# Performance work log

Hardware: AMD Instinct MI355X
Metric: run time of the kernel (lower is better)

The kernel has to match this reference:

```python
import jax, jax.numpy as jnp
import numpy as np

N = 65536   # total nodes
E = 1048576 # total edges (avg degree 16)
B = 512     # graphs in batch
H = 4       # gat1 heads
C = 64      # per-head channels / GNN_HIDDEN


def segment_softmax(logits, seg, num_segments):
    # numerically stable softmax over segments (PyG softmax semantics, eps=1e-16)
    m = jax.ops.segment_max(logits, seg, num_segments=num_segments)
    m = jnp.where(jnp.isfinite(m), m, 0.0)
    e = jnp.exp(logits - m[seg])
    s = jax.ops.segment_sum(e, seg, num_segments=num_segments)
    return e / (s[seg] + 1e-16)


def gat_conv(x, edge_index, edge_attr, W, att_src, att_dst, We, att_edge, bias, heads, out_ch, concat):
    # PyG GATConv with edge_dim, add_self_loops=False
    n = x.shape[0]
    h = (x @ W).reshape(n, heads, out_ch)                 # (N,H,C)
    src, dst = edge_index[0], edge_index[1]
    a_s = jnp.sum(h * att_src, axis=-1)                   # (N,H)
    a_d = jnp.sum(h * att_dst, axis=-1)                   # (N,H)
    he = (edge_attr @ We).reshape(-1, heads, out_ch)      # (E,H,C)
    a_e = jnp.sum(he * att_edge, axis=-1)                 # (E,H)
    alpha = jax.nn.leaky_relu(a_s[src] + a_d[dst] + a_e, negative_slope=0.2)
    alpha = segment_softmax(alpha, dst, n)                # softmax over incoming edges per dst
    out = jax.ops.segment_sum(h[src] * alpha[..., None], dst, num_segments=n)  # (N,H,C)
    out = out.reshape(n, heads * out_ch) if concat else out.mean(axis=1)
    return out + bias


def setup_inputs() -> dict:
    key = jax.random.key(0)
    ks = jax.random.split(key, 24)
    s = 0.05
    d = {}
    d["global_feat"] = jax.random.normal(ks[0], (B, 512), jnp.float32)
    d["x"] = jax.random.normal(ks[1], (N, 13), jnp.float32)
    d["roi_feats"] = jax.random.normal(ks[2], (N, 256), jnp.float32)
    d["edge_index"] = jax.random.randint(ks[3], (2, E), 0, N)
    d["edge_attr"] = jax.random.normal(ks[4], (E, 5), jnp.float32)
    d["batch_vec"] = jnp.sort(jax.random.randint(ks[5], (N,), 0, B))
    # roi_proj / scene_proj
    d["roi_W"] = jax.random.normal(ks[6], (256, 64), jnp.float32) * s
    d["roi_b"] = jnp.zeros((64,), jnp.float32)
    d["scene_W"] = jax.random.normal(ks[7], (512, 128), jnp.float32) * s
    d["scene_b"] = jnp.zeros((128,), jnp.float32)
    d["g1_W"] = jax.random.normal(ks[8], (77, H * C), jnp.float32) * s
    d["g1_att_src"] = jax.random.normal(ks[9], (H, C), jnp.float32) * s
    d["g1_att_dst"] = jax.random.normal(ks[10], (H, C), jnp.float32) * s
    d["g1_We"] = jax.random.normal(ks[11], (5, H * C), jnp.float32) * s
    d["g1_att_edge"] = jax.random.normal(ks[12], (H, C), jnp.float32) * s
    d["g1_bias"] = jnp.zeros((H * C,), jnp.float32)
    # gat2: 256 -> 64, 1 head
    d["g2_W"] = jax.random.normal(ks[13], (H * C, C), jnp.float32) * s
    d["g2_att_src"] = jax.random.normal(ks[14], (1, C), jnp.float32) * s
    d["g2_att_dst"] = jax.random.normal(ks[15], (1, C), jnp.float32) * s
    d["g2_We"] = jax.random.normal(ks[16], (5, C), jnp.float32) * s
    d["g2_att_edge"] = jax.random.normal(ks[17], (1, C), jnp.float32) * s
    d["g2_bias"] = jnp.zeros((C,), jnp.float32)
    # attention pooling gate + classifier
    d["gate_W"] = jax.random.normal(ks[18], (C, 1), jnp.float32) * s
    d["gate_b"] = jnp.zeros((1,), jnp.float32)
    d["cls1_W"] = jax.random.normal(ks[19], (128 + C, 64), jnp.float32) * s
    d["cls1_b"] = jnp.zeros((64,), jnp.float32)
    d["cls2_W"] = jax.random.normal(ks[20], (64, 3), jnp.float32) * s
    d["cls2_b"] = jnp.zeros((3,), jnp.float32)
    return d


def reference(global_feat, x, roi_feats, edge_index, edge_attr, batch_vec,
              roi_W, roi_b, scene_W, scene_b,
              g1_W, g1_att_src, g1_att_dst, g1_We, g1_att_edge, g1_bias,
              g2_W, g2_att_src, g2_att_dst, g2_We, g2_att_edge, g2_bias,
              gate_W, gate_b, cls1_W, cls1_b, cls2_W, cls2_b):
    scene = global_feat @ scene_W + scene_b                       # (B,128)
    vis = jax.nn.relu(roi_feats @ roi_W + roi_b)                  # (N,64)
    h = jnp.concatenate([x, vis], axis=-1)                        # (N,77)
    h = jax.nn.relu(gat_conv(h, edge_index, edge_attr, g1_W, g1_att_src, g1_att_dst, g1_We, g1_att_edge, g1_bias, H, C, True))
    h = gat_conv(h, edge_index, edge_attr, g2_W, g2_att_src, g2_att_dst, g2_We, g2_att_edge, g2_bias, 1, C, False)  # (N,64)
    # GlobalAttention pooling
    gate = segment_softmax((h @ gate_W + gate_b)[:, 0], batch_vec, B)
    rel = jax.ops.segment_sum(gate[:, None] * h, batch_vec, num_segments=B)  # (B,64)
    comb = jnp.concatenate([scene, rel], axis=-1)                 # (B,192)
    hid = jax.nn.relu(comb @ cls1_W + cls1_b)                     # dropout off (eval)
    return hid @ cls2_W + cls2_b                                  # (B,3)
```

## Files before the change

kernel.cpp:

```cpp
#include <hip/hip_runtime.h>

#define N_NODES 65536
#define N_EDGES 1048576
#define NB      512

typedef unsigned short u16;
typedef unsigned int   u32;
typedef unsigned long long u64;

__device__ __forceinline__ float bf2f(u16 u) { return __uint_as_float(((u32)u) << 16); }
__device__ __forceinline__ float lo16(u32 u) { return __uint_as_float(u << 16); }
__device__ __forceinline__ float hi16(u32 u) { return __uint_as_float(u & 0xffff0000u); }
__device__ __forceinline__ u16 f2bf(float f) {
    u32 u = __float_as_uint(f);
    u32 r = (u + 0x7fffu + ((u >> 16) & 1u)) >> 16;
    return (u16)r;
}
__device__ __forceinline__ float wsum(float v) {
    for (int o = 32; o; o >>= 1) v += __shfl_xor(v, o, 64);
    return v;
}
__device__ __forceinline__ float wmax(float v) {
    for (int o = 32; o; o >>= 1) v = fmaxf(v, __shfl_xor(v, o, 64));
    return v;
}

__global__ void k_prep(const float* g1We, const float* g1ae, const float* g2We, const float* g2ae,
                       float* M1, float* M2) {
    int t = threadIdx.x;
    if (t < 20) {
        int j = t >> 2, h = t & 3;
        float s = 0.f;
        for (int c = 0; c < 64; c++) s += g1We[j * 256 + h * 64 + c] * g1ae[h * 64 + c];
        M1[t] = s;
    } else if (t < 25) {
        int j = t - 20;
        float s = 0.f;
        for (int c = 0; c < 64; c++) s += g2We[j * 64 + c] * g2ae[c];
        M2[j] = s;
    }
}

__global__ __launch_bounds__(256) void k_scene(const float* __restrict__ gf, const float* __restrict__ W,
                                               const float* __restrict__ bias, float* __restrict__ scene) {
    int idx = blockIdx.x * 256 + threadIdx.x;
    int b = idx >> 7, j = idx & 127;
    float acc = 0.f;
    for (int k = 0; k < 512; k++) acc += gf[b * 512 + k] * W[k * 128 + j];
    scene[idx] = acc + bias[j];
}

__global__ __launch_bounds__(256) void k_hist(const int* ei, int* cnt) {
    int e = blockIdx.x * 256 + threadIdx.x;
    atomicAdd(&cnt[ei[N_EDGES + e]], 1);
}

__global__ __launch_bounds__(256) void k_scan_blk(const int* __restrict__ cnt, int* __restrict__ pre,
                                                  int* __restrict__ bsum) {
    __shared__ int sd[256];
    int t = threadIdx.x, b = blockIdx.x;
    int base = b * 1024 + t * 4;
    int4 c = *(const int4*)(cnt + base);
    int s = c.x + c.y + c.z + c.w;
    sd[t] = s;
    __syncthreads();
    for (int off = 1; off < 256; off <<= 1) {
        int v = (t >= off) ? sd[t - off] : 0;
        __syncthreads();
        sd[t] += v;
        __syncthreads();
    }
    int excl = sd[t] - s;
    int4 p;
    p.x = excl;
    p.y = excl + c.x;
    p.z = excl + c.x + c.y;
    p.w = excl + c.x + c.y + c.z;
    *(int4*)(pre + base) = p;
    if (t == 255) bsum[b] = sd[255];
}

__global__ __launch_bounds__(64) void k_scan_top(int* bsum) {
    int t = threadIdx.x;
    int v = bsum[t];
    int inc = v;
    for (int off = 1; off < 64; off <<= 1) {
        int u = __shfl_up(inc, off, 64);
        if (t >= off) inc += u;
    }
    bsum[t] = inc - v;
}

__global__ __launch_bounds__(256) void k_scan_fix(const int* __restrict__ pre, const int* __restrict__ bsum,
                                                  int* __restrict__ row_ptr, int* __restrict__ coarse_cur) {
    int i = blockIdx.x * 256 + threadIdx.x;
    int v = pre[i] + bsum[i >> 10];
    row_ptr[i] = v;
    if ((i & 255) == 0) coarse_cur[i >> 8] = v;
    if (i == 0) row_ptr[N_NODES] = N_EDGES;
}

__global__ __launch_bounds__(256) void k_bucket(const int* __restrict__ ei, int* coarse_cur,
                                                u32* __restrict__ bpack, int* __restrict__ bsrc) {
    __shared__ u32 stageP[4096];
    __shared__ int stageS[4096];
    __shared__ int bcnt[256], bscan[256], boff[256], gbase[256];
    int t = threadIdx.x;
    int e0 = blockIdx.x * 4096;
    bcnt[t] = 0;
    __syncthreads();
    int dreg[16], sreg[16];
    for (int it = 0; it < 16; it++) {
        int e = e0 + it * 256 + t;
        int dd = ei[N_EDGES + e];
        dreg[it] = dd;
        sreg[it] = ei[e];
        atomicAdd(&bcnt[dd >> 8], 1);
    }
    __syncthreads();
    int v = bcnt[t];
    bscan[t] = v;
    __syncthreads();
    for (int off = 1; off < 256; off <<= 1) {
        int u = (t >= off) ? bscan[t - off] : 0;
        __syncthreads();
        bscan[t] += u;
        __syncthreads();
    }
    boff[t] = bscan[t] - v;
    gbase[t] = v ? atomicAdd(&coarse_cur[t], v) : 0;
    __syncthreads();
    for (int it = 0; it < 16; it++) {
        int e = e0 + it * 256 + t;
        int b = dreg[it] >> 8;
        int pos = atomicAdd(&boff[b], 1);
        stageP[pos] = ((u32)e << 12) | (u32)(dreg[it] & 255);
        stageS[pos] = sreg[it];
    }
    __syncthreads();
    for (int idx = t; idx < 4096; idx += 256) {
        int lo = 0, hi = 255;
        while (lo < hi) { int mid = (lo + hi) >> 1; if (bscan[mid] > idx) hi = mid; else lo = mid + 1; }
        int b = lo;
        int g = gbase[b] + (idx - (bscan[b] - bcnt[b]));
        bpack[g] = stageP[idx];
        bsrc[g] = stageS[idx];
    }
}

__global__ __launch_bounds__(256) void k_sortb(const u32* __restrict__ bpack, const int* __restrict__ bsrc,
                                               const int* __restrict__ row_ptr,
                                               int* __restrict__ eord, int* __restrict__ ssrc) {
    __shared__ int cur[256];
    int t = threadIdx.x, b = blockIdx.x;
    int nbase = b * 256;
    cur[t] = row_ptr[nbase + t];
    __syncthreads();
    int beg = row_ptr[nbase];
    int end = row_ptr[nbase + 256];
    for (int i = beg + t; i < end; i += 256) {
        u32 wd = bpack[i];
        int src = bsrc[i];
        int d8 = wd & 255;
        int pos = atomicAdd(&cur[d8], 1);
        eord[pos] = (int)(wd >> 12);
        ssrc[pos] = src;
    }
}

__global__ __launch_bounds__(256) void k_payload(const int* __restrict__ eord, const float* __restrict__ ea,
                                                 const float* __restrict__ M1, const float* __restrict__ M2,
                                                 float* __restrict__ a1es, float* __restrict__ a2es) {
    int pos = blockIdx.x * 256 + threadIdx.x;
    int e = eord[pos];
    float v[5];
    for (int j = 0; j < 5; j++) v[j] = ea[(size_t)e * 5 + j];
    float4 o;
    o.x = v[0]*M1[0]  + v[1]*M1[4]  + v[2]*M1[8]  + v[3]*M1[12] + v[4]*M1[16];
    o.y = v[0]*M1[1]  + v[1]*M1[5]  + v[2]*M1[9]  + v[3]*M1[13] + v[4]*M1[17];
    o.z = v[0]*M1[2]  + v[1]*M1[6]  + v[2]*M1[10] + v[3]*M1[14] + v[4]*M1[18];
    o.w = v[0]*M1[3]  + v[1]*M1[7]  + v[2]*M1[11] + v[3]*M1[15] + v[4]*M1[19];
    *(float4*)(a1es + (size_t)pos * 4) = o;
    a2es[pos] = v[0]*M2[0] + v[1]*M2[1] + v[2]*M2[2] + v[3]*M2[3] + v[4]*M2[4];
}

__global__ __launch_bounds__(256) void k_vis(const float* __restrict__ A, const float* __restrict__ W,
                                             const float* __restrict__ bias, float* __restrict__ out) {
    __shared__ float At[64][68];
    __shared__ float Wl[64][68];
    int t = threadIdx.x;
    int n0 = blockIdx.x * 64;
    int cg = t & 15, rg = t >> 4;
    int sr = t >> 2, scs = (t & 3) * 16;
    float acc[4][4];
    for (int i = 0; i < 4; i++) for (int j = 0; j < 4; j++) acc[i][j] = 0.f;
    for (int kc = 0; kc < 4; kc++) {
        __syncthreads();
        const float* ap = A + (size_t)(n0 + sr) * 256 + kc * 64 + scs;
        float4 q0 = *(const float4*)ap, q1 = *(const float4*)(ap + 4);
        float4 q2 = *(const float4*)(ap + 8), q3 = *(const float4*)(ap + 12);
        At[scs + 0][sr] = q0.x;  At[scs + 1][sr] = q0.y;  At[scs + 2][sr] = q0.z;  At[scs + 3][sr] = q0.w;
        At[scs + 4][sr] = q1.x;  At[scs + 5][sr] = q1.y;  At[scs + 6][sr] = q1.z;  At[scs + 7][sr] = q1.w;
        At[scs + 8][sr] = q2.x;  At[scs + 9][sr] = q2.y;  At[scs + 10][sr] = q2.z; At[scs + 11][sr] = q2.w;
        At[scs + 12][sr] = q3.x; At[scs + 13][sr] = q3.y; At[scs + 14][sr] = q3.z; At[scs + 15][sr] = q3.w;
        const float* wp = W + (size_t)(kc * 64 + sr) * 64 + scs;
        *(float4*)&Wl[sr][scs + 0]  = *(const float4*)wp;
        *(float4*)&Wl[sr][scs + 4]  = *(const float4*)(wp + 4);
        *(float4*)&Wl[sr][scs + 8]  = *(const float4*)(wp + 8);
        *(float4*)&Wl[sr][scs + 12] = *(const float4*)(wp + 12);
        __syncthreads();
        for (int k = 0; k < 64; k++) {
            float4 a4 = *(const float4*)&At[k][rg * 4];
            float4 w4 = *(const float4*)&Wl[k][cg * 4];
            acc[0][0] += a4.x * w4.x; acc[0][1] += a4.x * w4.y; acc[0][2] += a4.x * w4.z; acc[0][3] += a4.x * w4.w;
            acc[1][0] += a4.y * w4.x; acc[1][1] += a4.y * w4.y; acc[1][2] += a4.y * w4.z; acc[1][3] += a4.y * w4.w;
            acc[2][0] += a4.z * w4.x; acc[2][1] += a4.z * w4.y; acc[2][2] += a4.z * w4.z; acc[2][3] += a4.z * w4.w;
            acc[3][0] += a4.w * w4.x; acc[3][1] += a4.w * w4.y; acc[3][2] += a4.w * w4.z; acc[3][3] += a4.w * w4.w;
        }
    }
    float4 bb = *(const float4*)(bias + cg * 4);
    for (int i = 0; i < 4; i++) {
        float4 o;
        o.x = fmaxf(acc[i][0] + bb.x, 0.f);
        o.y = fmaxf(acc[i][1] + bb.y, 0.f);
        o.z = fmaxf(acc[i][2] + bb.z, 0.f);
        o.w = fmaxf(acc[i][3] + bb.w, 0.f);
        *(float4*)(out + (size_t)(n0 + rg * 4 + i) * 64 + cg * 4) = o;
    }
}

__global__ __launch_bounds__(256) void k_h2(const u16* __restrict__ A, const float* __restrict__ W,
                                            const float* __restrict__ as_, const float* __restrict__ ad_,
                                            u16* __restrict__ out, float* __restrict__ a2s,
                                            float* __restrict__ a2d) {
    __shared__ float At[64][68];
    __shared__ float Wl[64][68];
    int t = threadIdx.x;
    int n0 = blockIdx.x * 64;
    int cg = t & 15, rg = t >> 4;
    int sr = t >> 2, scs = (t & 3) * 16;
    float acc[4][4];
    for (int i = 0; i < 4; i++) for (int j = 0; j < 4; j++) acc[i][j] = 0.f;
    for (int kc = 0; kc < 4; kc++) {
        __syncthreads();
        const u16* ap = A + (size_t)(n0 + sr) * 256 + kc * 64 + scs;
        uint4 u0 = *(const uint4*)ap;
        uint4 u1 = *(const uint4*)(ap + 8);
        At[scs + 0][sr] = lo16(u0.x);  At[scs + 1][sr] = hi16(u0.x);
        At[scs + 2][sr] = lo16(u0.y);  At[scs + 3][sr] = hi16(u0.y);
        At[scs + 4][sr] = lo16(u0.z);  At[scs + 5][sr] = hi16(u0.z);
        At[scs + 6][sr] = lo16(u0.w);  At[scs + 7][sr] = hi16(u0.w);
        At[scs + 8][sr] = lo16(u1.x);  At[scs + 9][sr] = hi16(u1.x);
        At[scs + 10][sr] = lo16(u1.y); At[scs + 11][sr] = hi16(u1.y);
        At[scs + 12][sr] = lo16(u1.z); At[scs + 13][sr] = hi16(u1.z);
        At[scs + 14][sr] = lo16(u1.w); At[scs + 15][sr] = hi16(u1.w);
        const float* wp = W + (size_t)(kc * 64 + sr) * 64 + scs;
        *(float4*)&Wl[sr][scs + 0]  = *(const float4*)wp;
        *(float4*)&Wl[sr][scs + 4]  = *(const float4*)(wp + 4);
        *(float4*)&Wl[sr][scs + 8]  = *(const float4*)(wp + 8);
        *(float4*)&Wl[sr][scs + 12] = *(const float4*)(wp + 12);
        __syncthreads();
        for (int k = 0; k < 64; k++) {
            float4 a4 = *(const float4*)&At[k][rg * 4];
            float4 w4 = *(const float4*)&Wl[k][cg * 4];
            acc[0][0] += a4.x * w4.x; acc[0][1] += a4.x * w4.y; acc[0][2] += a4.x * w4.z; acc[0][3] += a4.x * w4.w;
            acc[1][0] += a4.y * w4.x; acc[1][1] += a4.y * w4.y; acc[1][2] += a4.y * w4.z; acc[1][3] += a4.y * w4.w;
            acc[2][0] += a4.z * w4.x; acc[2][1] += a4.z * w4.y; acc[2][2] += a4.z * w4.z; acc[2][3] += a4.z * w4.w;
            acc[3][0] += a4.w * w4.x; acc[3][1] += a4.w * w4.y; acc[3][2] += a4.w * w4.z; acc[3][3] += a4.w * w4.w;
        }
    }
    u32* outu = (u32*)out;
    for (int i = 0; i < 4; i++) {
        uint2 pk;
        pk.x = (u32)f2bf(acc[i][0]) | ((u32)f2bf(acc[i][1]) << 16);
        pk.y = (u32)f2bf(acc[i][2]) | ((u32)f2bf(acc[i][3]) << 16);
        *(uint2*)(outu + (size_t)(n0 + rg * 4 + i) * 32 + cg * 2) = pk;
    }
    float4 as4 = *(const float4*)(as_ + cg * 4);
    float4 ad4 = *(const float4*)(ad_ + cg * 4);
    #pragma unroll
    for (int i = 0; i < 4; i++) {
        float ps = acc[i][0] * as4.x + acc[i][1] * as4.y + acc[i][2] * as4.z + acc[i][3] * as4.w;
        float pd = acc[i][0] * ad4.x + acc[i][1] * ad4.y + acc[i][2] * ad4.z + acc[i][3] * ad4.w;
        for (int o = 1; o < 16; o <<= 1) { ps += __shfl_xor(ps, o, 64); pd += __shfl_xor(pd, o, 64); }
        if (cg == 0) {
            a2s[n0 + rg * 4 + i] = ps;
            a2d[n0 + rg * 4 + i] = pd;
        }
    }
}

__global__ __launch_bounds__(256) void k_h1(const float* __restrict__ x, const float* __restrict__ vis,
                                            const float* __restrict__ g1W, u16* __restrict__ h1) {
    __shared__ float At[77][36];
    __shared__ float Wl[77][132];
    int t = threadIdx.x, ch = blockIdx.y;
    int n0 = blockIdx.x * 32;
    int cg = t & 31, rg = t >> 5;
    for (int idx = t; idx < 9856; idx += 256) {
        int k = idx >> 7, c = idx & 127;
        Wl[k][c] = g1W[(size_t)k * 256 + ch * 128 + c];
    }
    for (int idx = t; idx < 2464; idx += 256) {
        int r = idx / 77, k = idx - r * 77;
        At[k][r] = (k < 13) ? x[(size_t)(n0 + r) * 13 + k] : vis[(size_t)(n0 + r) * 64 + (k - 13)];
    }
    __syncthreads();
    float acc[4][4];
    for (int i = 0; i < 4; i++) for (int j = 0; j < 4; j++) acc[i][j] = 0.f;
    for (int k = 0; k < 77; k++) {
        float4 a4 = *(const float4*)&At[k][rg * 4];
        float4 w4 = *(const float4*)&Wl[k][cg * 4];
        acc[0][0] += a4.x * w4.x; acc[0][1] += a4.x * w4.y; acc[0][2] += a4.x * w4.z; acc[0][3] += a4.x * w4.w;
        acc[1][0] += a4.y * w4.x; acc[1][1] += a4.y * w4.y; acc[1][2] += a4.y * w4.z; acc[1][3] += a4.y * w4.w;
        acc[2][0] += a4.z * w4.x; acc[2][1] += a4.z * w4.y; acc[2][2] += a4.z * w4.z; acc[2][3] += a4.z * w4.w;
        acc[3][0] += a4.w * w4.x; acc[3][1] += a4.w * w4.y; acc[3][2] += a4.w * w4.z; acc[3][3] += a4.w * w4.w;
    }
    for (int i = 0; i < 4; i++) {
        uint2 pk;
        pk.x = (u32)f2bf(acc[i][0]) | ((u32)f2bf(acc[i][1]) << 16);
        pk.y = (u32)f2bf(acc[i][2]) | ((u32)f2bf(acc[i][3]) << 16);
        *(uint2*)(h1 + (size_t)(n0 + rg * 4 + i) * 256 + ch * 128 + cg * 4) = pk;
    }
}

__global__ __launch_bounds__(256) void k_a1(const u16* __restrict__ h1, const float* __restrict__ as_,
                                            const float* __restrict__ ad_, float* a1s, float* a1d) {
    int t = threadIdx.x;
    int w = t >> 6, L = t & 63;
    float4 as4 = *(const float4*)(as_ + 4 * L);
    float4 ad4 = *(const float4*)(ad_ + 4 * L);
    int base = (blockIdx.x * 4 + w) * 16;
    for (int j = 0; j < 16; j++) {
        int n = base + j;
        uint2 u = *((const uint2*)(h1 + (size_t)n * 256) + L);
        float v0 = lo16(u.x), v1 = hi16(u.x), v2 = lo16(u.y), v3 = hi16(u.y);
        float ps = v0 * as4.x + v1 * as4.y + v2 * as4.z + v3 * as4.w;
        float pd = v0 * ad4.x + v1 * ad4.y + v2 * ad4.z + v3 * ad4.w;
        for (int o = 1; o < 16; o <<= 1) { ps += __shfl_xor(ps, o, 64); pd += __shfl_xor(pd, o, 64); }
        if ((L & 15) == 0) {
            a1s[n * 4 + (L >> 4)] = ps;
            a1d[n * 4 + (L >> 4)] = pd;
        }
    }
}

__global__ __launch_bounds__(256) void k_soft1(const int* __restrict__ row_ptr, const int* __restrict__ ssrc,
                                               const float* __restrict__ a1s, const float* __restrict__ a1d,
                                               const float* __restrict__ a1es, float* __restrict__ w1) {
    int t = threadIdx.x;
    int wv = t >> 6, L = t & 63;
    int n = blockIdx.x * 4 + wv;
    int h = L >> 4, j = L & 15;
    int beg = row_ptr[n], deg = row_ptr[n + 1] - beg;
    if (deg == 0) return;
    float adn = a1d[n * 4 + h];
    float m = -3.0e38f, s = 0.f;
    for (int i = j; i < deg; i += 16) {
        int pos = beg + i;
        float l = a1s[ssrc[pos] * 4 + h] + adn + a1es[(size_t)pos * 4 + h];
        l = (l > 0.f) ? l : 0.2f * l;
        w1[(size_t)pos * 4 + h] = l;
        if (l > m) { s = s * __expf(m - l) + 1.f; m = l; }
        else       { s += __expf(l - m); }
    }
    for (int o = 1; o < 16; o <<= 1) {
        float mo = __shfl_xor(m, o, 64), so = __shfl_xor(s, o, 64);
        float M = fmaxf(m, mo);
        s = s * __expf(m - M) + so * __expf(mo - M);
        m = M;
    }
    float inv = 1.f / (s + 1e-16f);
    for (int i = j; i < deg; i += 16) {
        int pos = beg + i;
        float l = w1[(size_t)pos * 4 + h];
        w1[(size_t)pos * 4 + h] = __expf(l - m) * inv;
    }
}

__global__ __launch_bounds__(256) void k_gath1(const int* __restrict__ row_ptr, const int* __restrict__ ssrc,
                                               const float* __restrict__ w1, const u16* __restrict__ h1,
                                               const float* __restrict__ bias, u16* __restrict__ out1) {
    int t = threadIdx.x;
    int wv = t >> 6, L = t & 63;
    int n = blockIdx.x * 4 + wv;
    int beg = row_ptr[n], deg = row_ptr[n + 1] - beg;
    int halfE = L >> 5;
    int L32 = L & 31;
    int hd = L32 >> 3;
    float acc[8];
    #pragma unroll
    for (int j = 0; j < 8; j++) acc[j] = 0.f;
    int last = beg + deg - 1;
    for (int i = 0; i < deg; i += 8) {
        int iA = i + halfE, iB = i + 2 + halfE, iC = i + 4 + halfE, iD = i + 6 + halfE;
        bool vA = iA < deg, vB = iB < deg, vC = iC < deg, vD = iD < deg;
        int cA = vA ? beg + iA : last, cB = vB ? beg + iB : last;
        int cC = vC ? beg + iC : last, cD = vD ? beg + iD : last;
        int sA = ssrc[cA], sB = ssrc[cB], sC = ssrc[cC], sD = ssrc[cD];
        float wA = vA ? w1[(size_t)cA * 4 + hd] : 0.f;
        float wB = vB ? w1[(size_t)cB * 4 + hd] : 0.f;
        float wC = vC ? w1[(size_t)cC * 4 + hd] : 0.f;
        float wD = vD ? w1[(size_t)cD * 4 + hd] : 0.f;
        uint4 uA = *((const uint4*)(h1 + (size_t)sA * 256) + L32);
        uint4 uB = *((const uint4*)(h1 + (size_t)sB * 256) + L32);
        uint4 uC = *((const uint4*)(h1 + (size_t)sC * 256) + L32);
        uint4 uD = *((const uint4*)(h1 + (size_t)sD * 256) + L32);
        acc[0] += wA * lo16(uA.x) + wB * lo16(uB.x) + wC * lo16(uC.x) + wD * lo16(uD.x);
        acc[1] += wA * hi16(uA.x) + wB * hi16(uB.x) + wC * hi16(uC.x) + wD * hi16(uD.x);
        acc[2] += wA * lo16(uA.y) + wB * lo16(uB.y) + wC * lo16(uC.y) + wD * lo16(uD.y);
        acc[3] += wA * hi16(uA.y) + wB * hi16(uB.y) + wC * hi16(uC.y) + wD * hi16(uD.y);
        acc[4] += wA * lo16(uA.z) + wB * lo16(uB.z) + wC * lo16(uC.z) + wD * lo16(uD.z);
        acc[5] += wA * hi16(uA.z) + wB * hi16(uB.z) + wC * hi16(uC.z) + wD * hi16(uD.z);
        acc[6] += wA * lo16(uA.w) + wB * lo16(uB.w) + wC * lo16(uC.w) + wD * lo16(uD.w);
        acc[7] += wA * hi16(uA.w) + wB * hi16(uB.w) + wC * hi16(uC.w) + wD * hi16(uD.w);
    }
    #pragma unroll
    for (int j = 0; j < 8; j++) acc[j] += __shfl_xor(acc[j], 32, 64);
    if (halfE == 0) {
        float4 b0 = *(const float4*)(bias + 8 * L32);
        float4 b1 = *(const float4*)(bias + 8 * L32 + 4);
        uint4 pk;
        pk.x = (u32)f2bf(fmaxf(acc[0] + b0.x, 0.f)) | ((u32)f2bf(fmaxf(acc[1] + b0.y, 0.f)) << 16);
        pk.y = (u32)f2bf(fmaxf(acc[2] + b0.z, 0.f)) | ((u32)f2bf(fmaxf(acc[3] + b0.w, 0.f)) << 16);
        pk.z = (u32)f2bf(fmaxf(acc[4] + b1.x, 0.f)) | ((u32)f2bf(fmaxf(acc[5] + b1.y, 0.f)) << 16);
        pk.w = (u32)f2bf(fmaxf(acc[6] + b1.z, 0.f)) | ((u32)f2bf(fmaxf(acc[7] + b1.w, 0.f)) << 16);
        *((uint4*)(out1 + (size_t)n * 256) + L32) = pk;
    }
}

__global__ __launch_bounds__(256) void k_soft2(const int* __restrict__ row_ptr, const int* __restrict__ ssrc,
                                               const float* __restrict__ a2s, const float* __restrict__ a2d,
                                               const float* __restrict__ a2es, float* __restrict__ w2) {
    int t = threadIdx.x;
    int wv = t >> 6, L = t & 63;
    int g = L >> 4, j = L & 15;
    int n = blockIdx.x * 16 + wv * 4 + g;
    int beg = row_ptr[n], deg = row_ptr[n + 1] - beg;
    if (deg == 0) return;
    float adn = a2d[n];
    float m = -3.0e38f, s = 0.f;
    for (int i = j; i < deg; i += 16) {
        int pos = beg + i;
        float l = a2s[ssrc[pos]] + adn + a2es[pos];
        l = (l > 0.f) ? l : 0.2f * l;
        w2[pos] = l;
        if (l > m) { s = s * __expf(m - l) + 1.f; m = l; }
        else       { s += __expf(l - m); }
    }
    for (int o = 1; o < 16; o <<= 1) {
        float mo = __shfl_xor(m, o, 64), so = __shfl_xor(s, o, 64);
        float M = fmaxf(m, mo);
        s = s * __expf(m - M) + so * __expf(mo - M);
        m = M;
    }
    float inv = 1.f / (s + 1e-16f);
    for (int i = j; i < deg; i += 16) {
        int pos = beg + i;
        float l = w2[pos];
        w2[pos] = __expf(l - m) * inv;
    }
}

__global__ __launch_bounds__(256) void k_gath2(const int* __restrict__ row_ptr, const int* __restrict__ ssrc,
                                               const float* __restrict__ w2, const u16* __restrict__ h2b,
                                               const float* __restrict__ bias, float* __restrict__ hfin) {
    int t = threadIdx.x;
    int wv = t >> 6, L = t & 63;
    int n = blockIdx.x * 4 + wv;
    int beg = row_ptr[n], deg = row_ptr[n + 1] - beg;
    int halfE = L >> 5;
    int L32 = L & 31;
    float a0 = 0.f, a1v = 0.f;
    int last = beg + deg - 1;
    const u32* h2u = (const u32*)h2b;
    for (int i = 0; i < deg; i += 8) {
        int iA = i + halfE, iB = i + 2 + halfE, iC = i + 4 + halfE, iD = i + 6 + halfE;
        bool vA = iA < deg, vB = iB < deg, vC = iC < deg, vD = iD < deg;
        int cA = vA ? beg + iA : last, cB = vB ? beg + iB : last;
        int cC = vC ? beg + iC : last, cD = vD ? beg + iD : last;
        int sA = ssrc[cA], sB = ssrc[cB], sC = ssrc[cC], sD = ssrc[cD];
        float wA = vA ? w2[cA] : 0.f;
        float wB = vB ? w2[cB] : 0.f;
        float wC = vC ? w2[cC] : 0.f;
        float wD = vD ? w2[cD] : 0.f;
        u32 uA = h2u[(size_t)sA * 32 + L32];
        u32 uB = h2u[(size_t)sB * 32 + L32];
        u32 uC = h2u[(size_t)sC * 32 + L32];
        u32 uD = h2u[(size_t)sD * 32 + L32];
        a0  += wA * lo16(uA) + wB * lo16(uB) + wC * lo16(uC) + wD * lo16(uD);
        a1v += wA * hi16(uA) + wB * hi16(uB) + wC * hi16(uC) + wD * hi16(uD);
    }
    a0  += __shfl_xor(a0, 32, 64);
    a1v += __shfl_xor(a1v, 32, 64);
    if (halfE == 0) {
        float2 o;
        o.x = a0  + bias[2 * L32];
        o.y = a1v + bias[2 * L32 + 1];
        *(float2*)(hfin + (size_t)n * 64 + 2 * L32) = o;
    }
}

__global__ __launch_bounds__(64) void k_pool(const int* __restrict__ bvec, const float* __restrict__ hf,
                                             const float* gateW, const float* gateb,
                                             const float* __restrict__ scene,
                                             const float* c1W, const float* c1b,
                                             const float* c2W, const float* c2b,
                                             float* __restrict__ outp) {
    int b = blockIdx.x, lane = threadIdx.x;
    __shared__ float gwl[64], se[64], comb[192], hid[64];
    gwl[lane] = gateW[lane];
    __syncthreads();
    int s0, s1;
    { int lo = 0, hi = N_NODES; while (lo < hi) { int mid = (lo + hi) >> 1; if (bvec[mid] < b) lo = mid + 1; else hi = mid; } s0 = lo; }
    { int lo = 0, hi = N_NODES; while (lo < hi) { int mid = (lo + hi) >> 1; if (bvec[mid] < b + 1) lo = mid + 1; else hi = mid; } s1 = lo; }
    float gb = gateb[0];
    float m = -3.0e38f, ssum = 0.f, acc = 0.f;
    for (int cs = s0; cs < s1; cs += 64) {
        int cnt = min(64, s1 - cs);
        float l = -3.0e38f;
        if (lane < cnt) {
            int n = cs + lane;
            float d = 0.f;
            for (int i = 0; i < 64; i++) d += hf[(size_t)n * 64 + i] * gwl[i];
            l = d + gb;
        }
        float cm = wmax(l);
        float newm = fmaxf(m, cm);
        float rsc = __expf(m - newm);
        float e = (lane < cnt) ? __expf(l - newm) : 0.f;
        float es = wsum(e);
        ssum = ssum * rsc + es;
        se[lane] = e;
        __syncthreads();
        float a2 = 0.f;
        for (int i = 0; i < cnt; i++) a2 += se[i] * hf[(size_t)(cs + i) * 64 + lane];
        acc = acc * rsc + a2;
        __syncthreads();
        m = newm;
    }
    float rel = acc / (ssum + 1e-16f);
    comb[lane] = scene[b * 128 + lane];
    comb[64 + lane] = scene[b * 128 + 64 + lane];
    comb[128 + lane] = rel;
    __syncthreads();
    float hj = 0.f;
    for (int k = 0; k < 192; k++) hj += comb[k] * c1W[k * 64 + lane];
    hj += c1b[lane];
    hid[lane] = fmaxf(hj, 0.f);
    __syncthreads();
    if (lane < 3) {
        float o = 0.f;
        for (int k = 0; k < 64; k++) o += hid[k] * c2W[k * 3 + lane];
        o += c2b[lane];
        outp[b * 3 + lane] = o;
    }
}

extern "C" void kernel_launch(void* const* d_in, const int* in_sizes, int n_in,
                              void* d_out, int out_size, void* d_ws, size_t ws_size,
                              hipStream_t stream) {
    (void)in_sizes; (void)n_in; (void)out_size; (void)ws_size;
    const float* gf     = (const float*)d_in[0];
    const float* x      = (const float*)d_in[1];
    const float* roi    = (const float*)d_in[2];
    const int*   ei     = (const int*)d_in[3];
    const float* ea     = (const float*)d_in[4];
    const int*   bvec   = (const int*)d_in[5];
    const float* roiW   = (const float*)d_in[6];
    const float* roib   = (const float*)d_in[7];
    const float* sceneW = (const float*)d_in[8];
    const float* sceneb = (const float*)d_in[9];
    const float* g1W    = (const float*)d_in[10];
    const float* g1as   = (const float*)d_in[11];
    const float* g1ad   = (const float*)d_in[12];
    const float* g1We   = (const float*)d_in[13];
    const float* g1ae   = (const float*)d_in[14];
    const float* g1b    = (const float*)d_in[15];
    const float* g2W    = (const float*)d_in[16];
    const float* g2as   = (const float*)d_in[17];
    const float* g2ad   = (const float*)d_in[18];
    const float* g2We   = (const float*)d_in[19];
    const float* g2ae   = (const float*)d_in[20];
    const float* g2b    = (const float*)d_in[21];
    const float* gateW  = (const float*)d_in[22];
    const float* gateb  = (const float*)d_in[23];
    const float* c1W    = (const float*)d_in[24];
    const float* c1b    = (const float*)d_in[25];
    const float* c2W    = (const float*)d_in[26];
    const float* c2b    = (const float*)d_in[27];

    char* w = (char*)d_ws;
    size_t o = 0;
    auto nxt = [&](size_t bytes) -> char* {
        char* p = w + o;
        o += (bytes + 255) & ~(size_t)255;
        return p;
    };
    float* scene  = (float*)nxt((size_t)NB * 128 * 4);
    float* M1     = (float*)nxt(80);
    float* M2     = (float*)nxt(32);
    int* cnt      = (int*)nxt((size_t)N_NODES * 4);
    int* pre      = (int*)nxt((size_t)N_NODES * 4);
    int* bsum     = (int*)nxt(64 * 4);
    int* row_ptr  = (int*)nxt((size_t)(N_NODES + 1) * 4);
    int* coarse   = (int*)nxt(256 * 4);
    u32* bpack    = (u32*)nxt((size_t)N_EDGES * 4);
    int* bsrc     = (int*)nxt((size_t)N_EDGES * 4);
    int* eord     = (int*)nxt((size_t)N_EDGES * 4);
    int* ssrc     = (int*)nxt((size_t)N_EDGES * 4);
    float* a1es   = (float*)nxt((size_t)N_EDGES * 16);
    float* a2es   = (float*)nxt((size_t)N_EDGES * 4);
    float* visbuf = (float*)nxt((size_t)N_NODES * 64 * 4);
    u16* h1       = (u16*)nxt((size_t)N_NODES * 256 * 2);
    u16* out1     = (u16*)nxt((size_t)N_NODES * 256 * 2);
    float* w1buf  = (float*)nxt((size_t)N_EDGES * 16);
    float* hfin   = (float*)nxt((size_t)N_NODES * 64 * 4);
    float* a1s    = (float*)nxt((size_t)N_NODES * 16);
    float* a1d    = (float*)nxt((size_t)N_NODES * 16);
    float* a2s    = (float*)nxt((size_t)N_NODES * 4);
    float* a2d    = (float*)nxt((size_t)N_NODES * 4);

    float* vis = visbuf;
    float* w2  = visbuf;
    float* w1  = w1buf;
    u16*   h2b = (u16*)w1buf;

    hipMemsetAsync(cnt, 0, (size_t)N_NODES * 4, stream);
    k_prep<<<1, 32, 0, stream>>>(g1We, g1ae, g2We, g2ae, M1, M2);
    k_scene<<<(NB * 128) / 256, 256, 0, stream>>>(gf, sceneW, sceneb, scene);
    k_hist<<<N_EDGES / 256, 256, 0, stream>>>(ei, cnt);
    k_scan_blk<<<64, 256, 0, stream>>>(cnt, pre, bsum);
    k_scan_top<<<1, 64, 0, stream>>>(bsum);
    k_scan_fix<<<N_NODES / 256, 256, 0, stream>>>(pre, bsum, row_ptr, coarse);
    k_bucket<<<256, 256, 0, stream>>>(ei, coarse, bpack, bsrc);
    k_sortb<<<256, 256, 0, stream>>>(bpack, bsrc, row_ptr, eord, ssrc);
    k_payload<<<N_EDGES / 256, 256, 0, stream>>>(eord, ea, M1, M2, a1es, a2es);
    k_vis<<<N_NODES / 64, 256, 0, stream>>>(roi, roiW, roib, vis);
    k_h1<<<dim3(N_NODES / 32, 2), 256, 0, stream>>>(x, vis, g1W, h1);
    k_a1<<<N_NODES / 64, 256, 0, stream>>>(h1, g1as, g1ad, a1s, a1d);
    k_soft1<<<N_NODES / 4, 256, 0, stream>>>(row_ptr, ssrc, a1s, a1d, a1es, w1);
    k_gath1<<<N_NODES / 4, 256, 0, stream>>>(row_ptr, ssrc, w1, h1, g1b, out1);
    k_h2<<<N_NODES / 64, 256, 0, stream>>>(out1, g2W, g2as, g2ad, h2b, a2s, a2d);
    k_soft2<<<N_NODES / 16, 256, 0, stream>>>(row_ptr, ssrc, a2s, a2d, a2es, w2);
    k_gath2<<<N_NODES / 4, 256, 0, stream>>>(row_ptr, ssrc, w2, h2b, g2b, hfin);
    k_pool<<<NB, 64, 0, stream>>>(bvec, hfin, gateW, gateb, scene, c1W, c1b, c2W, c2b, (float*)d_out);
}
```

Measured before the change: 624.8 us.

## Fuse attention dots into h1 GEMM and defer softmax normalization to gather

Computes the per-head source/destination attention scores in k_h1's epilogue from the fp32 accumulators, which removes the separate k_a1 kernel and its re-read of h1. The softmax kernels now store only the raw logits plus a per-node (max, 1/sum) pair instead of doing a second pass that rewrites every edge weight. The gather kernels recompute exp(l-m)*inv on the fly. This saves one kernel launch and a read-modify-write pass over the edge weight arrays, at the cost of extra exp work in the gathers and a small extra per-node buffer.

```diff
diff --git a/kernel.cpp b/kernel.cpp
--- a/kernel.cpp
+++ b/kernel.cpp
@@ -291,7 +291,10 @@
 }
 
 __global__ __launch_bounds__(256) void k_h1(const float* __restrict__ x, const float* __restrict__ vis,
-                                            const float* __restrict__ g1W, u16* __restrict__ h1) {
+                                            const float* __restrict__ g1W,
+                                            const float* __restrict__ as_, const float* __restrict__ ad_,
+                                            u16* __restrict__ h1, float* __restrict__ a1s,
+                                            float* __restrict__ a1d) {
     __shared__ float At[77][36];
     __shared__ float Wl[77][132];
     int t = threadIdx.x, ch = blockIdx.y;
@@ -322,32 +325,27 @@
         pk.y = (u32)f2bf(acc[i][2]) | ((u32)f2bf(acc[i][3]) << 16);
         *(uint2*)(h1 + (size_t)(n0 + rg * 4 + i) * 256 + ch * 128 + cg * 4) = pk;
     }
-}
-
-__global__ __launch_bounds__(256) void k_a1(const u16* __restrict__ h1, const float* __restrict__ as_,
-                                            const float* __restrict__ ad_, float* a1s, float* a1d) {
-    int t = threadIdx.x;
-    int w = t >> 6, L = t & 63;
-    float4 as4 = *(const float4*)(as_ + 4 * L);
-    float4 ad4 = *(const float4*)(ad_ + 4 * L);
-    int base = (blockIdx.x * 4 + w) * 16;
-    for (int j = 0; j < 16; j++) {
-        int n = base + j;
-        uint2 u = *((const uint2*)(h1 + (size_t)n * 256) + L);
-        float v0 = lo16(u.x), v1 = hi16(u.x), v2 = lo16(u.y), v3 = hi16(u.y);
-        float ps = v0 * as4.x + v1 * as4.y + v2 * as4.z + v3 * as4.w;
-        float pd = v0 * ad4.x + v1 * ad4.y + v2 * ad4.z + v3 * ad4.w;
+    int gh = ch * 2 + (cg >> 4);
+    int co = (cg & 15) * 4;
+    float4 as4 = *(const float4*)(as_ + gh * 64 + co);
+    float4 ad4 = *(const float4*)(ad_ + gh * 64 + co);
+    #pragma unroll
+    for (int i = 0; i < 4; i++) {
+        float ps = acc[i][0] * as4.x + acc[i][1] * as4.y + acc[i][2] * as4.z + acc[i][3] * as4.w;
+        float pd = acc[i][0] * ad4.x + acc[i][1] * ad4.y + acc[i][2] * ad4.z + acc[i][3] * ad4.w;
         for (int o = 1; o < 16; o <<= 1) { ps += __shfl_xor(ps, o, 64); pd += __shfl_xor(pd, o, 64); }
-        if ((L & 15) == 0) {
-            a1s[n * 4 + (L >> 4)] = ps;
-            a1d[n * 4 + (L >> 4)] = pd;
+        if ((cg & 15) == 0) {
+            int n = n0 + rg * 4 + i;
+            a1s[n * 4 + gh] = ps;
+            a1d[n * 4 + gh] = pd;
         }
     }
 }
 
 __global__ __launch_bounds__(256) void k_soft1(const int* __restrict__ row_ptr, const int* __restrict__ ssrc,
                                                const float* __restrict__ a1s, const float* __restrict__ a1d,
-                                               const float* __restrict__ a1es, float* __restrict__ w1) {
+                                               const float* __restrict__ a1es, float* __restrict__ w1,
+                                               float2* __restrict__ minv1) {
     int t = threadIdx.x;
     int wv = t >> 6, L = t & 63;
     int n = blockIdx.x * 4 + wv;
@@ -370,16 +368,12 @@
         s = s * __expf(m - M) + so * __expf(mo - M);
         m = M;
     }
-    float inv = 1.f / (s + 1e-16f);
-    for (int i = j; i < deg; i += 16) {
-        int pos = beg + i;
-        float l = w1[(size_t)pos * 4 + h];
-        w1[(size_t)pos * 4 + h] = __expf(l - m) * inv;
-    }
+    if (j == 0) minv1[n * 4 + h] = make_float2(m, 1.f / (s + 1e-16f));
 }
 
 __global__ __launch_bounds__(256) void k_gath1(const int* __restrict__ row_ptr, const int* __restrict__ ssrc,
-                                               const float* __restrict__ w1, const u16* __restrict__ h1,
+                                               const float* __restrict__ w1, const float2* __restrict__ minv1,
+                                               const u16* __restrict__ h1,
                                                const float* __restrict__ bias, u16* __restrict__ out1) {
     int t = threadIdx.x;
     int wv = t >> 6, L = t & 63;
@@ -388,6 +382,7 @@
     int halfE = L >> 5;
     int L32 = L & 31;
     int hd = L32 >> 3;
+    float2 mi = (deg > 0) ? minv1[n * 4 + hd] : make_float2(0.f, 0.f);
     float acc[8];
     #pragma unroll
     for (int j = 0; j < 8; j++) acc[j] = 0.f;
@@ -398,10 +393,14 @@
         int cA = vA ? beg + iA : last, cB = vB ? beg + iB : last;
         int cC = vC ? beg + iC : last, cD = vD ? beg + iD : last;
         int sA = ssrc[cA], sB = ssrc[cB], sC = ssrc[cC], sD = ssrc[cD];
-        float wA = vA ? w1[(size_t)cA * 4 + hd] : 0.f;
-        float wB = vB ? w1[(size_t)cB * 4 + hd] : 0.f;
-        float wC = vC ? w1[(size_t)cC * 4 + hd] : 0.f;
-        float wD = vD ? w1[(size_t)cD * 4 + hd] : 0.f;
+        float lA = w1[(size_t)cA * 4 + hd];
+        float lB = w1[(size_t)cB * 4 + hd];
+        float lC = w1[(size_t)cC * 4 + hd];
+        float lD = w1[(size_t)cD * 4 + hd];
+        float wA = vA ? __expf(lA - mi.x) * mi.y : 0.f;
+        float wB = vB ? __expf(lB - mi.x) * mi.y : 0.f;
+        float wC = vC ? __expf(lC - mi.x) * mi.y : 0.f;
+        float wD = vD ? __expf(lD - mi.x) * mi.y : 0.f;
         uint4 uA = *((const uint4*)(h1 + (size_t)sA * 256) + L32);
         uint4 uB = *((const uint4*)(h1 + (size_t)sB * 256) + L32);
         uint4 uC = *((const uint4*)(h1 + (size_t)sC * 256) + L32);
@@ -431,7 +430,8 @@
 
 __global__ __launch_bounds__(256) void k_soft2(const int* __restrict__ row_ptr, const int* __restrict__ ssrc,
                                                const float* __restrict__ a2s, const float* __restrict__ a2d,
-                                               const float* __restrict__ a2es, float* __restrict__ w2) {
+                                               const float* __restrict__ a2es, float* __restrict__ w2,
+                                               float2* __restrict__ minv2) {
     int t = threadIdx.x;
     int wv = t >> 6, L = t & 63;
     int g = L >> 4, j = L & 15;
@@ -454,16 +454,12 @@
         s = s * __expf(m - M) + so * __expf(mo - M);
         m = M;
     }
-    float inv = 1.f / (s + 1e-16f);
-    for (int i = j; i < deg; i += 16) {
-        int pos = beg + i;
-        float l = w2[pos];
-        w2[pos] = __expf(l - m) * inv;
-    }
+    if (j == 0) minv2[n] = make_float2(m, 1.f / (s + 1e-16f));
 }
 
 __global__ __launch_bounds__(256) void k_gath2(const int* __restrict__ row_ptr, const int* __restrict__ ssrc,
-                                               const float* __restrict__ w2, const u16* __restrict__ h2b,
+                                               const float* __restrict__ w2, const float2* __restrict__ minv2,
+                                               const u16* __restrict__ h2b,
                                                const float* __restrict__ bias, float* __restrict__ hfin) {
     int t = threadIdx.x;
     int wv = t >> 6, L = t & 63;
@@ -471,6 +467,7 @@
     int beg = row_ptr[n], deg = row_ptr[n + 1] - beg;
     int halfE = L >> 5;
     int L32 = L & 31;
+    float2 mi = (deg > 0) ? minv2[n] : make_float2(0.f, 0.f);
     float a0 = 0.f, a1v = 0.f;
     int last = beg + deg - 1;
     const u32* h2u = (const u32*)h2b;
@@ -480,10 +477,11 @@
         int cA = vA ? beg + iA : last, cB = vB ? beg + iB : last;
         int cC = vC ? beg + iC : last, cD = vD ? beg + iD : last;
         int sA = ssrc[cA], sB = ssrc[cB], sC = ssrc[cC], sD = ssrc[cD];
-        float wA = vA ? w2[cA] : 0.f;
-        float wB = vB ? w2[cB] : 0.f;
-        float wC = vC ? w2[cC] : 0.f;
-        float wD = vD ? w2[cD] : 0.f;
+        float lA = w2[cA], lB = w2[cB], lC = w2[cC], lD = w2[cD];
+        float wA = vA ? __expf(lA - mi.x) * mi.y : 0.f;
+        float wB = vB ? __expf(lB - mi.x) * mi.y : 0.f;
+        float wC = vC ? __expf(lC - mi.x) * mi.y : 0.f;
+        float wD = vD ? __expf(lD - mi.x) * mi.y : 0.f;
         u32 uA = h2u[(size_t)sA * 32 + L32];
         u32 uB = h2u[(size_t)sB * 32 + L32];
         u32 uC = h2u[(size_t)sC * 32 + L32];
@@ -620,6 +618,8 @@
     float* a1d    = (float*)nxt((size_t)N_NODES * 16);
     float* a2s    = (float*)nxt((size_t)N_NODES * 4);
     float* a2d    = (float*)nxt((size_t)N_NODES * 4);
+    float2* minv1 = (float2*)nxt((size_t)N_NODES * 4 * 8);
+    float2* minv2 = (float2*)nxt((size_t)N_NODES * 8);
 
     float* vis = visbuf;
     float* w2  = visbuf;
@@ -637,12 +637,11 @@
     k_sortb<<<256, 256, 0, stream>>>(bpack, bsrc, row_ptr, eord, ssrc);
     k_payload<<<N_EDGES / 256, 256, 0, stream>>>(eord, ea, M1, M2, a1es, a2es);
     k_vis<<<N_NODES / 64, 256, 0, stream>>>(roi, roiW, roib, vis);
-    k_h1<<<dim3(N_NODES / 32, 2), 256, 0, stream>>>(x, vis, g1W, h1);
-    k_a1<<<N_NODES / 64, 256, 0, stream>>>(h1, g1as, g1ad, a1s, a1d);
-    k_soft1<<<N_NODES / 4, 256, 0, stream>>>(row_ptr, ssrc, a1s, a1d, a1es, w1);
-    k_gath1<<<N_NODES / 4, 256, 0, stream>>>(row_ptr, ssrc, w1, h1, g1b, out1);
+    k_h1<<<dim3(N_NODES / 32, 2), 256, 0, stream>>>(x, vis, g1W, g1as, g1ad, h1, a1s, a1d);
+    k_soft1<<<N_NODES / 4, 256, 0, stream>>>(row_ptr, ssrc, a1s, a1d, a1es, w1, minv1);
+    k_gath1<<<N_NODES / 4, 256, 0, stream>>>(row_ptr, ssrc, w1, minv1, h1, g1b, out1);
     k_h2<<<N_NODES / 64, 256, 0, stream>>>(out1, g2W, g2as, g2ad, h2b, a2s, a2d);
-    k_soft2<<<N_NODES / 16, 256, 0, stream>>>(row_ptr, ssrc, a2s, a2d, a2es, w2);
-    k_gath2<<<N_NODES / 4, 256, 0, stream>>>(row_ptr, ssrc, w2, h2b, g2b, hfin);
+    k_soft2<<<N_NODES / 16, 256, 0, stream>>>(row_ptr, ssrc, a2s, a2d, a2es, w2, minv2);
+    k_gath2<<<N_NODES / 4, 256, 0, stream>>>(row_ptr, ssrc, w2, minv2, h2b, g2b, hfin);
     k_pool<<<NB, 64, 0, stream>>>(bvec, hfin, gateW, gateb, scene, c1W, c1b, c2W, c2b, (float*)d_out);
 }
```

Result: faster. 612.0 us (-2.1%).
